# Optimization experiments

Measured on AMD Instinct MI355X. Metric: run time of the kernel, lower is better.

## Reference

```python
import jax, jax.numpy as jnp
import numpy as np

N = 262144
C = 81
NUM_HARD = 32768


def setup_inputs() -> dict:
    key = jax.random.key(0)
    k1, k2, k3, k4 = jax.random.split(key, 4)
    return {
        "cls_score": jax.random.normal(k1, (N, C), dtype=jnp.float32),
        "rois_label": jax.random.randint(k2, (N,), 0, C, dtype=jnp.int32),
        "bbox_pred": jax.random.normal(k3, (N, 4), dtype=jnp.float32),
        "rois_target": jax.random.normal(k4, (N, 4), dtype=jnp.float32),
        "rois_inside_ws": jnp.ones((N, 4), dtype=jnp.float32),
        "rois_outside_ws": jnp.ones((N, 4), dtype=jnp.float32),
        "num_hard": NUM_HARD,
    }


def reference(cls_score, rois_label, bbox_pred, rois_target,
              rois_inside_ws, rois_outside_ws, num_hard):
    num_classes = cls_score.shape[1]
    pos = rois_label > 0                                   # [N] bool
    num_pos = jnp.sum(pos.astype(jnp.float32))

    # --- hard-example mining on detached scores (no grad through selection) ---
    conf_p = jax.lax.stop_gradient(cls_score)              # [N, C]
    x_max = jnp.max(conf_p)                                # global scalar max (as in torch code)
    lse = jnp.log(jnp.sum(jnp.exp(conf_p - x_max), axis=1)) + x_max   # [N]
    gathered = jnp.take_along_axis(conf_p, rois_label[:, None].astype(jnp.int32), axis=1)[:, 0]
    loss_c = lse - gathered                                # [N]
    loss_c = jnp.where(pos, jnp.float32(100.0), loss_c)    # force positives in
    _, topk_idx = jax.lax.top_k(loss_c, num_hard)          # [num_hard]

    # --- weighted cross entropy on selected hard examples ---
    weight = jnp.ones((num_classes,), dtype=jnp.float32).at[0].set(num_pos / num_hard)
    sel_logits = cls_score[topk_idx]                       # [num_hard, C]
    sel_labels = rois_label[topk_idx]                      # [num_hard]
    logp = jax.nn.log_softmax(sel_logits, axis=1)
    nll = -jnp.take_along_axis(logp, sel_labels[:, None].astype(jnp.int32), axis=1)[:, 0]
    w = weight[sel_labels]
    loss_cls = jnp.sum(w * nll) / jnp.sum(w)               # torch weighted-mean CE

    # --- smooth L1 on positive rois only (masked; mean over num_pos*4 elems) ---
    diff = bbox_pred - rois_target                         # [N, 4]
    ad = jnp.abs(diff)
    sl1 = jnp.where(ad < 1.0, 0.5 * diff * diff, ad - 0.5)
    posf = pos.astype(sl1.dtype)[:, None]
    loss_box = jnp.sum(sl1 * posf) / (num_pos * 4.0)

    return loss_cls, loss_box
```

## Files before the change

kernel.cpp:

```cpp
#include <hip/hip_runtime.h>

#define NROWS 262144
#define NCLS  81
#define NTILES 4096
#define TILE_FLOATS 5184
#define KEY100 0xC2C80000u

__device__ __forceinline__ unsigned mono(float f) {
    unsigned u = __float_as_uint(f);
    return (u & 0x80000000u) ? ~u : (u | 0x80000000u);
}

__device__ __forceinline__ void gload_lds16(const void* g, void* l) {
    __builtin_amdgcn_global_load_lds(
        (const __attribute__((address_space(1))) unsigned int*)g,
        (__attribute__((address_space(3))) unsigned int*)l,
        16, 0, 0);
}

__global__ __launch_bounds__(256) void row_kernel(
        const float* __restrict__ cls, const int* __restrict__ label,
        const float* __restrict__ bpred, const float* __restrict__ btgt,
        float4* __restrict__ partial)
{
    __shared__ float sm[TILE_FLOATS];

    const int t = threadIdx.x;
    const int lane = t & 63, wid = t >> 6;
    const int blk = blockIdx.x;

    const int gi = blk*256 + t;
    const float pbox = bpred[gi], qbox = btgt[gi];
    const int rowh1 = wid*16 + (lane >> 3);
    const int rowh2 = rowh1 + 8;
    const int lblA = label[blk*64 + rowh1];
    const int lblB = label[blk*64 + rowh2];
    const int lblBox = label[blk*64 + (t >> 2)];

    {
        const float4* srcA = (const float4*)(cls + (size_t)blk * TILE_FLOATS) + wid*324;
        float4* dstA = (float4*)sm + wid*324;
        gload_lds16((const void*)(srcA + lane),       (void*)(dstA));
        gload_lds16((const void*)(srcA + 64 + lane),  (void*)(dstA + 64));
        if (lane < 34)
            gload_lds16((const void*)(srcA + 128 + lane), (void*)(dstA + 128));
        const float4* srcB = srcA + 162;
        float4* dstB = dstA + 162;
        gload_lds16((const void*)(srcB + lane),       (void*)(dstB));
        gload_lds16((const void*)(srcB + 64 + lane),  (void*)(dstB + 64));
        if (lane < 34)
            gload_lds16((const void*)(srcB + 128 + lane), (void*)(dstB + 128));
    }

    const int j = lane & 7;
    unsigned pcnt = 0, gcnt = 0, ecnt = 0;
    float gtv = 0.f, pnv = 0.f;

    asm volatile("s_waitcnt vmcnt(3)" ::: "memory");
    __builtin_amdgcn_sched_barrier(0);
    {
        const float* rp = sm + rowh1 * NCLS;
        float s = 0.f;
        #pragma unroll
        for (int i = 0; i < 10; ++i) s += __expf(rp[j + 8*i]);
        if (j == 0) s += __expf(rp[80]);
        s += __shfl_xor(s, 1); s += __shfl_xor(s, 2); s += __shfl_xor(s, 4);
        if (j == 0) {
            float nll = __logf(s) - rp[lblA];
            bool pos = lblA > 0;
            unsigned kk = mono(pos ? 100.0f : nll);
            pcnt += pos ? 1u : 0u;
            gcnt += (kk > KEY100) ? 1u : 0u;
            ecnt += (!pos && kk == KEY100) ? 1u : 0u;
            gtv  += (kk > KEY100) ? nll : 0.f;
            pnv  += pos ? nll : 0.f;
        }
    }

    asm volatile("s_waitcnt vmcnt(0)" ::: "memory");
    __builtin_amdgcn_sched_barrier(0);
    {
        const float* rp = sm + rowh2 * NCLS;
        float s = 0.f;
        #pragma unroll
        for (int i = 0; i < 10; ++i) s += __expf(rp[j + 8*i]);
        if (j == 0) s += __expf(rp[80]);
        s += __shfl_xor(s, 1); s += __shfl_xor(s, 2); s += __shfl_xor(s, 4);
        if (j == 0) {
            float nll = __logf(s) - rp[lblB];
            bool pos = lblB > 0;
            unsigned kk = mono(pos ? 100.0f : nll);
            pcnt += pos ? 1u : 0u;
            gcnt += (kk > KEY100) ? 1u : 0u;
            ecnt += (!pos && kk == KEY100) ? 1u : 0u;
            gtv  += (kk > KEY100) ? nll : 0.f;
            pnv  += pos ? nll : 0.f;
        }
    }

    float bsum = 0.f;
    if (lblBox > 0) {
        float d = pbox - qbox, ad = fabsf(d);
        bsum = (ad < 1.f) ? 0.5f*d*d : ad - 0.5f;
    }

    unsigned cnt = pcnt | (gcnt << 8) | (ecnt << 16);
    #pragma unroll
    for (int off = 32; off; off >>= 1) {
        cnt  += __shfl_xor(cnt, off);
        gtv  += __shfl_xor(gtv, off);
        pnv  += __shfl_xor(pnv, off);
        bsum += __shfl_xor(bsum, off);
    }
    if (lane == 0)
        partial[blk*4 + wid] = make_float4(__uint_as_float(cnt), gtv, pnv, bsum);
}

__device__ void scan_desc_64k_1024(const unsigned* hist, unsigned k,
                                   unsigned* outB, unsigned* outRem,
                                   unsigned* wsum )
{
    const int t = threadIdx.x, lane = t & 63, wid = t >> 6;
    unsigned sum = 0;
    for (int j = 0; j < 64; ++j) sum += hist[65535 - (t*64 + j)];
    unsigned inc = sum;
    #pragma unroll
    for (int off = 1; off < 64; off <<= 1) {
        unsigned v = __shfl_up(inc, off);
        if (lane >= off) inc += v;
    }
    if (lane == 63) wsum[wid] = inc;
    __syncthreads();
    unsigned woff = 0;
    for (int w = 0; w < wid; ++w) woff += wsum[w];
    unsigned running = woff + inc - sum;
    for (int j = 0; j < 64; ++j) {
        unsigned bkt = 65535u - (unsigned)(t*64 + j);
        unsigned c = hist[bkt];
        if (running < k && running + c >= k) { *outB = bkt; *outRem = k - running; }
        running += c;
    }
}

__global__ __launch_bounds__(1024) void finalize_kernel(
        const float* __restrict__ cls, const int* __restrict__ label,
        const float4* __restrict__ partial, const int* __restrict__ d_num_hard,
        unsigned* __restrict__ hist, float* __restrict__ nllbuf,
        float* __restrict__ out)
{
    const int t = threadIdx.x, lane = t & 63, wid = t >> 6;
    __shared__ unsigned wNp[16], wNg[16], wNe[16];
    __shared__ float wPn[16], wGt[16], wBx[16];
    __shared__ unsigned sCross, sCumBefore;
    __shared__ float sFull, sPartial;
    __shared__ float sm[TILE_FLOATS];
    __shared__ float snll[64];
    __shared__ int slbl[64];

    unsigned npI[4]; float pnI[4];
    unsigned npS = 0, ngS = 0, neS = 0;
    float gtS = 0.f, pnS = 0.f, bxS = 0.f;
    #pragma unroll
    for (int i = 0; i < 4; ++i) {
        unsigned npw = 0, ngw = 0, new_ = 0; float gtw = 0.f, pnw = 0.f, bxw = 0.f;
        #pragma unroll
        for (int w2 = 0; w2 < 4; ++w2) {
            float4 v = partial[(size_t)(t*4 + i)*4 + w2];
            unsigned c = __float_as_uint(v.x);
            npw += c & 255u; ngw += (c >> 8) & 255u; new_ += (c >> 16) & 255u;
            gtw += v.y; pnw += v.z; bxw += v.w;
        }
        npI[i] = npw; pnI[i] = pnw;
        npS += npw; ngS += ngw; neS += new_;
        gtS += gtw; pnS += pnw; bxS += bxw;
    }
    unsigned incNp = npS; float incPn = pnS;
    #pragma unroll
    for (int off = 1; off < 64; off <<= 1) {
        unsigned v = __shfl_up(incNp, off);
        float    f = __shfl_up(incPn, off);
        if (lane >= off) { incNp += v; incPn += f; }
    }
    #pragma unroll
    for (int off = 32; off; off >>= 1) {
        ngS += __shfl_xor(ngS, off); neS += __shfl_xor(neS, off);
        gtS += __shfl_xor(gtS, off); bxS += __shfl_xor(bxS, off);
    }
    if (lane == 63) { wNp[wid] = incNp; wPn[wid] = incPn; }
    if (lane == 0)  { wNg[wid] = ngS; wNe[wid] = neS; wGt[wid] = gtS; wBx[wid] = bxS; }
    __syncthreads();

    unsigned NP = 0, NG = 0, NE = 0; float GT = 0.f, BX = 0.f;
    unsigned npOff = 0; float pnOff = 0.f;
    for (int w = 0; w < 16; ++w) {
        NP += wNp[w]; NG += wNg[w]; NE += wNe[w]; GT += wGt[w]; BX += wBx[w];
        if (w < wid) { npOff += wNp[w]; pnOff += wPn[w]; }
    }
    const unsigned k = (unsigned)(*d_num_hard);
    const bool fast = (NG < k) && (NG + NP >= k) && (NE == 0);

    if (fast) {
        const unsigned need = k - NG;
        unsigned cum = npOff + incNp - npS;
        float    fl  = pnOff + incPn - pnS;
        #pragma unroll
        for (int i = 0; i < 4; ++i) {
            if (cum < need && cum + npI[i] >= need) {
                sCross = (unsigned)(t*4 + i); sCumBefore = cum; sFull = fl;
            }
            cum += npI[i]; fl += pnI[i];
        }
        __syncthreads();

        {
            const float4* src = (const float4*)(cls + (size_t)sCross * TILE_FLOATS);
            float4* dst = (float4*)sm;
            dst[t] = src[t];
            if (t < 272) dst[t + 1024] = src[t + 1024];
            if (t < 64) slbl[t] = label[(int)sCross*64 + t];
        }
        __syncthreads();

        {
            const int brow = t >> 4, bj = t & 15;
            const float* rp = sm + brow * NCLS;
            float s = 0.f;
            for (int i = bj; i < NCLS; i += 16) s += __expf(rp[i]);
            s += __shfl_xor(s, 1);
            s += __shfl_xor(s, 2);
            s += __shfl_xor(s, 4);
            s += __shfl_xor(s, 8);
            if (bj == 0) snll[brow] = __logf(s) - rp[slbl[brow]];
        }
        __syncthreads();

        if (t < 64) {
            int lbl = slbl[t];
            bool pos = lbl > 0;
            unsigned long long m = __ballot(pos);
            unsigned rank = (unsigned)__popcll(m & ((1ull << t) - 1ull));
            unsigned rem = need - sCumBefore;
            float c = (pos && rank < rem) ? snll[t] : 0.f;
            #pragma unroll
            for (int off = 32; off; off >>= 1) c += __shfl_xor(c, off);
            if (t == 0) sPartial = c;
        }
        __syncthreads();
        if (t == 0) {
            float wgt0 = (float)NP / (float)k;
            out[0] = (wgt0*GT + sFull + sPartial) / (wgt0*NG + (float)need);
            out[1] = BX / ((float)NP * 4.0f);
        }
        return;
    }

    __shared__ unsigned wsum[16];
    __shared__ unsigned sB1, sKrem, sTkey, sNeed;
    __shared__ unsigned wEq[16];
    __shared__ float r1[16], r2[16];
    __syncthreads();

    for (int r = t; r < NROWS; r += 1024) {
        const float* rp = cls + (size_t)r * NCLS;
        float ssum = 0.f;
        for (int cix = 0; cix < NCLS; ++cix) ssum += __expf(rp[cix]);
        nllbuf[r] = __logf(ssum) - rp[label[r]];
    }
    __syncthreads();

    for (int i = t; i < 65536; i += 1024) hist[i] = 0u;
    __syncthreads();
    for (int base = 0; base < NROWS; base += 1024) {
        int r = base + t;
        unsigned key = mono(label[r] > 0 ? 100.0f : nllbuf[r]);
        unsigned bkt = key >> 16;
        unsigned long long active = __ballot(1);
        while (active) {
            int leader = (int)__builtin_ctzll(active);
            unsigned lb = __shfl(bkt, leader);
            unsigned long long grp = __ballot(bkt == lb) & active;
            if (lane == leader) atomicAdd(&hist[lb], (unsigned)__popcll(grp));
            active &= ~grp;
        }
    }
    __syncthreads();
    scan_desc_64k_1024(hist, k, &sB1, &sKrem, wsum);
    __syncthreads();

    for (int i = t; i < 65536; i += 1024) hist[i] = 0u;
    __syncthreads();
    for (int base = 0; base < NROWS; base += 1024) {
        int r = base + t;
        unsigned key = mono(label[r] > 0 ? 100.0f : nllbuf[r]);
        bool in = (key >> 16) == sB1;
        unsigned bkt = key & 0xFFFFu;
        unsigned long long active = __ballot(in);
        while (active) {
            int leader = (int)__builtin_ctzll(active);
            unsigned lb = __shfl(bkt, leader);
            unsigned long long grp = __ballot(in && bkt == lb) & active;
            if (lane == leader) atomicAdd(&hist[lb], (unsigned)__popcll(grp));
            active &= ~grp;
        }
    }
    __syncthreads();
    scan_desc_64k_1024(hist, sKrem, &sTkey, &sNeed, wsum);
    __syncthreads();
    if (t == 0) sTkey = (sB1 << 16) | sTkey;
    __syncthreads();

    const unsigned tkey = sTkey, need = sNeed;
    const float wgt0 = (float)NP / (float)k;
    float accN = 0.f, accW = 0.f;
    unsigned running = 0;
    for (int base = 0; base < NROWS; base += 1024) {
        int r = base + t;
        int lbl = label[r]; float v = nllbuf[r];
        unsigned key = mono(lbl > 0 ? 100.0f : v);
        bool eq = (key == tkey);
        unsigned long long b = __ballot(eq);
        if (lane == 0) wEq[wid] = (unsigned)__popcll(b);
        __syncthreads();
        unsigned woff = 0, chunkTotal = 0;
        for (int w = 0; w < 16; ++w) {
            chunkTotal += wEq[w];
            if (w < wid) woff += wEq[w];
        }
        unsigned rank = running + woff + (unsigned)__popcll(b & ((1ull << lane) - 1ull));
        bool sel = (key > tkey) || (eq && rank < need);
        if (sel) { float wg = (lbl == 0) ? wgt0 : 1.f; accN += wg * v; accW += wg; }
        running += chunkTotal;
        __syncthreads();
    }
    #pragma unroll
    for (int off = 32; off; off >>= 1) {
        accN += __shfl_xor(accN, off);
        accW += __shfl_xor(accW, off);
    }
    if (lane == 0) { r1[wid] = accN; r2[wid] = accW; }
    __syncthreads();
    if (t == 0) {
        float N = 0.f, W = 0.f;
        for (int w = 0; w < 16; ++w) { N += r1[w]; W += r2[w]; }
        out[0] = N / W;
        out[1] = BX / ((float)NP * 4.0f);
    }
}

extern "C" void kernel_launch(void* const* d_in, const int* in_sizes, int n_in,
                              void* d_out, int out_size, void* d_ws, size_t ws_size,
                              hipStream_t stream) {
    const float* cls   = (const float*)d_in[0];
    const int*   label = (const int*)d_in[1];
    const float* bpred = (const float*)d_in[2];
    const float* btgt  = (const float*)d_in[3];
    const int*   nh    = (const int*)d_in[6];
    float* out = (float*)d_out;

    char* ws = (char*)d_ws;
    float4*   partial = (float4*)(ws);
    unsigned* hist    = (unsigned*)(ws + 262144);
    float*    nllbuf  = (float*)(ws + 524288);

    row_kernel<<<NTILES, 256, 0, stream>>>(cls, label, bpred, btgt, partial);
    finalize_kernel<<<1, 1024, 0, stream>>>(cls, label, partial, nh,
                                            hist, nllbuf, out);
}
```

Measured before the change: 33.17 us.

## Process two row tiles per block with double LDS buffers and 4-lane row reduction

Each block now handles two 64-row tiles, staging them into separate LDS buffers. The second tile's loads stay in flight while the first is reduced, and the grid is halved. Each row is now reduced by 4 lanes instead of 8, so every thread does more exponentials and fewer shuffles. This doubles LDS use per block, which may lower occupancy, and lengthens each thread's serial work.

```diff
diff --git a/kernel.cpp b/kernel.cpp
--- a/kernel.cpp
+++ b/kernel.cpp
@@ -23,97 +23,103 @@
         const float* __restrict__ bpred, const float* __restrict__ btgt,
         float4* __restrict__ partial)
 {
-    __shared__ float sm[TILE_FLOATS];
+    __shared__ float smA[TILE_FLOATS];
+    __shared__ float smB[TILE_FLOATS];
 
     const int t = threadIdx.x;
     const int lane = t & 63, wid = t >> 6;
-    const int blk = blockIdx.x;
-
-    const int gi = blk*256 + t;
-    const float pbox = bpred[gi], qbox = btgt[gi];
-    const int rowh1 = wid*16 + (lane >> 3);
-    const int rowh2 = rowh1 + 8;
-    const int lblA = label[blk*64 + rowh1];
-    const int lblB = label[blk*64 + rowh2];
-    const int lblBox = label[blk*64 + (t >> 2)];
+    const int tileA = blockIdx.x * 2;
+    const int tileB = tileA + 1;
+    const int trow = lane >> 2;
+    const int j    = lane & 3;
+    const int rowl = wid*16 + trow;
+
+    const float pbA = bpred[tileA*256 + t], qbA = btgt[tileA*256 + t];
+    const float pbB = bpred[tileB*256 + t], qbB = btgt[tileB*256 + t];
+    const int lblA   = label[tileA*64 + rowl];
+    const int lblB   = label[tileB*64 + rowl];
+    const int lblBxA = label[tileA*64 + (t >> 2)];
+    const int lblBxB = label[tileB*64 + (t >> 2)];
+    __builtin_amdgcn_sched_barrier(0);
 
     {
-        const float4* srcA = (const float4*)(cls + (size_t)blk * TILE_FLOATS) + wid*324;
-        float4* dstA = (float4*)sm + wid*324;
-        gload_lds16((const void*)(srcA + lane),       (void*)(dstA));
-        gload_lds16((const void*)(srcA + 64 + lane),  (void*)(dstA + 64));
-        if (lane < 34)
-            gload_lds16((const void*)(srcA + 128 + lane), (void*)(dstA + 128));
-        const float4* srcB = srcA + 162;
-        float4* dstB = dstA + 162;
-        gload_lds16((const void*)(srcB + lane),       (void*)(dstB));
-        gload_lds16((const void*)(srcB + 64 + lane),  (void*)(dstB + 64));
-        if (lane < 34)
-            gload_lds16((const void*)(srcB + 128 + lane), (void*)(dstB + 128));
-    }
-
-    const int j = lane & 7;
-    unsigned pcnt = 0, gcnt = 0, ecnt = 0;
-    float gtv = 0.f, pnv = 0.f;
-
-    asm volatile("s_waitcnt vmcnt(3)" ::: "memory");
+        const float4* srcA = (const float4*)cls + (size_t)tileA*1296 + wid*324;
+        float4* dstA = (float4*)smA + wid*324;
+        #pragma unroll
+        for (int r = 0; r < 5; ++r)
+            gload_lds16((const void*)(srcA + r*64 + lane), (void*)(dstA + r*64));
+        if (lane < 4)
+            gload_lds16((const void*)(srcA + 320 + lane), (void*)(dstA + 320));
+    }
     __builtin_amdgcn_sched_barrier(0);
     {
-        const float* rp = sm + rowh1 * NCLS;
+        const float4* srcB = (const float4*)cls + (size_t)tileB*1296 + wid*324;
+        float4* dstB = (float4*)smB + wid*324;
+        #pragma unroll
+        for (int r = 0; r < 5; ++r)
+            gload_lds16((const void*)(srcB + r*64 + lane), (void*)(dstB + r*64));
+        if (lane < 4)
+            gload_lds16((const void*)(srcB + 320 + lane), (void*)(dstB + 320));
+    }
+
+    float bsA = 0.f, bsB = 0.f;
+    if (lblBxA > 0) { float d = pbA - qbA, ad = fabsf(d); bsA = (ad < 1.f) ? 0.5f*d*d : ad - 0.5f; }
+    if (lblBxB > 0) { float d = pbB - qbB, ad = fabsf(d); bsB = (ad < 1.f) ? 0.5f*d*d : ad - 0.5f; }
+
+    unsigned cntA = 0, cntB = 0;
+    float gtA = 0.f, pnA = 0.f, gtB = 0.f, pnB = 0.f;
+
+    asm volatile("s_waitcnt vmcnt(6)" ::: "memory");
+    __builtin_amdgcn_sched_barrier(0);
+    {
+        const float* rp = smA + rowl * NCLS;
         float s = 0.f;
         #pragma unroll
-        for (int i = 0; i < 10; ++i) s += __expf(rp[j + 8*i]);
+        for (int i = 0; i < 20; ++i) s += __expf(rp[j + 4*i]);
         if (j == 0) s += __expf(rp[80]);
-        s += __shfl_xor(s, 1); s += __shfl_xor(s, 2); s += __shfl_xor(s, 4);
+        s += __shfl_xor(s, 1); s += __shfl_xor(s, 2);
         if (j == 0) {
             float nll = __logf(s) - rp[lblA];
             bool pos = lblA > 0;
             unsigned kk = mono(pos ? 100.0f : nll);
-            pcnt += pos ? 1u : 0u;
-            gcnt += (kk > KEY100) ? 1u : 0u;
-            ecnt += (!pos && kk == KEY100) ? 1u : 0u;
-            gtv  += (kk > KEY100) ? nll : 0.f;
-            pnv  += pos ? nll : 0.f;
+            cntA = (pos ? 1u : 0u) | ((kk > KEY100 ? 1u : 0u) << 8)
+                 | (((!pos && kk == KEY100) ? 1u : 0u) << 16);
+            gtA = (kk > KEY100) ? nll : 0.f;
+            pnA = pos ? nll : 0.f;
         }
     }
 
     asm volatile("s_waitcnt vmcnt(0)" ::: "memory");
     __builtin_amdgcn_sched_barrier(0);
     {
-        const float* rp = sm + rowh2 * NCLS;
+        const float* rp = smB + rowl * NCLS;
         float s = 0.f;
         #pragma unroll
-        for (int i = 0; i < 10; ++i) s += __expf(rp[j + 8*i]);
+        for (int i = 0; i < 20; ++i) s += __expf(rp[j + 4*i]);
         if (j == 0) s += __expf(rp[80]);
-        s += __shfl_xor(s, 1); s += __shfl_xor(s, 2); s += __shfl_xor(s, 4);
+        s += __shfl_xor(s, 1); s += __shfl_xor(s, 2);
         if (j == 0) {
             float nll = __logf(s) - rp[lblB];
             bool pos = lblB > 0;
             unsigned kk = mono(pos ? 100.0f : nll);
-            pcnt += pos ? 1u : 0u;
-            gcnt += (kk > KEY100) ? 1u : 0u;
-            ecnt += (!pos && kk == KEY100) ? 1u : 0u;
-            gtv  += (kk > KEY100) ? nll : 0.f;
-            pnv  += pos ? nll : 0.f;
-        }
-    }
-
-    float bsum = 0.f;
-    if (lblBox > 0) {
-        float d = pbox - qbox, ad = fabsf(d);
-        bsum = (ad < 1.f) ? 0.5f*d*d : ad - 0.5f;
-    }
-
-    unsigned cnt = pcnt | (gcnt << 8) | (ecnt << 16);
+            cntB = (pos ? 1u : 0u) | ((kk > KEY100 ? 1u : 0u) << 8)
+                 | (((!pos && kk == KEY100) ? 1u : 0u) << 16);
+            gtB = (kk > KEY100) ? nll : 0.f;
+            pnB = pos ? nll : 0.f;
+        }
+    }
+
     #pragma unroll
     for (int off = 32; off; off >>= 1) {
-        cnt  += __shfl_xor(cnt, off);
-        gtv  += __shfl_xor(gtv, off);
-        pnv  += __shfl_xor(pnv, off);
-        bsum += __shfl_xor(bsum, off);
-    }
-    if (lane == 0)
-        partial[blk*4 + wid] = make_float4(__uint_as_float(cnt), gtv, pnv, bsum);
+        cntA += __shfl_xor(cntA, off); gtA += __shfl_xor(gtA, off);
+        pnA  += __shfl_xor(pnA, off);  bsA += __shfl_xor(bsA, off);
+        cntB += __shfl_xor(cntB, off); gtB += __shfl_xor(gtB, off);
+        pnB  += __shfl_xor(pnB, off);  bsB += __shfl_xor(bsB, off);
+    }
+    if (lane == 0) {
+        partial[tileA*4 + wid] = make_float4(__uint_as_float(cntA), gtA, pnA, bsA);
+        partial[tileB*4 + wid] = make_float4(__uint_as_float(cntB), gtB, pnB, bsB);
+    }
 }
 
 __device__ void scan_desc_64k_1024(const unsigned* hist, unsigned k,
@@ -362,7 +368,7 @@
     unsigned* hist    = (unsigned*)(ws + 262144);
     float*    nllbuf  = (float*)(ws + 524288);
 
-    row_kernel<<<NTILES, 256, 0, stream>>>(cls, label, bpred, btgt, partial);
+    row_kernel<<<NTILES/2, 256, 0, stream>>>(cls, label, bpred, btgt, partial);
     finalize_kernel<<<1, 1024, 0, stream>>>(cls, label, partial, nh,
                                             hist, nllbuf, out);
 }
```

Result: no change. 33.14 us (-0.1%).
